# Optimization experiments

Hardware: AMD Instinct MI355X
Metric: run time of the kernel (lower is better)

## Reference

```python
import jax, jax.numpy as jnp
import numpy as np

ALPHA = 0.03
RETURN_WEIGHT = 0.6
SHARPE_WEIGHT = 0.4
WINDOW = 20  # min(20, N//4) == 20 for N = 2**21
N = 2097152


def setup_inputs() -> dict:
    key = jax.random.key(0)
    k1, k2 = jax.random.split(key)
    predictions = jax.random.normal(k1, (N, 1), dtype=jnp.float32)
    returns = jax.random.normal(k2, (N,), dtype=jnp.float32) * 0.02  # daily-return scale
    return {"predictions": predictions, "returns": returns}


def _std(x):
    # torch.std uses the unbiased estimator (ddof=1)
    return jnp.std(x, ddof=1)


def _forward(predictions, returns):
    signals = jnp.tanh(predictions)                 # [N, 1]
    r = returns * signals.squeeze(-1)               # [N] portfolio returns
    n = r.shape[0]

    mean_return = jnp.mean(r)
    std_return = _std(r) + 1e-8
    base_sharpe = mean_return / std_return

    # Rolling std over trailing WINDOW (vectorized form of the python loop):
    # window k covers r[k : k+WINDOW], k in [0, n-WINDOW)
    win = jnp.stack([r[j:n - WINDOW + j] for j in range(WINDOW)], axis=-1)  # [n-W, W]
    rolling_vol = jnp.std(win, axis=-1, ddof=1)
    vol_stability = 1.0 / (_std(rolling_vol) + 1e-6)
    enhanced_sharpe = base_sharpe * (1.0 + 0.1 * vol_stability)

    return_magnitude = jnp.mean(jnp.abs(r))
    positive_frequency = jnp.mean((r > 0).astype(r.dtype))

    dr = r[1:] - r[:-1]
    return_smoothness = 1.0 / (jnp.mean(jnp.abs(dr)) + 1e-6)
    momentum_consistency = jnp.mean(jnp.sign(r[1:]) * jnp.sign(r[:-1]))

    cum = jnp.cumsum(r)
    running_max = jax.lax.cummax(cum, axis=0)
    max_drawdown = jnp.max(running_max - cum)
    drawdown_penalty = jax.nn.relu(max_drawdown - 0.05)

    sorted_r = jnp.sort(r)
    cvar_samples = max(1, int(n * ALPHA))
    cvar = -jnp.mean(sorted_r[:cvar_samples])

    ds = signals[1:] - signals[:-1]
    signal_changes = jnp.mean(jnp.abs(ds))
    signal_smoothness = 1.0 / (signal_changes + 1e-6)

    sharpe_components = (0.4 * enhanced_sharpe
                         + 0.25 * return_magnitude
                         + 0.15 * positive_frequency
                         + 0.1 * momentum_consistency
                         + 0.05 * return_smoothness
                         + 0.05 * signal_smoothness)
    risk_penalties = 0.05 * cvar + 0.02 * drawdown_penalty + 0.01 * signal_changes

    return -(RETURN_WEIGHT * return_magnitude
             + SHARPE_WEIGHT * sharpe_components
             - risk_penalties)


def reference(predictions, returns):
    return _forward(predictions, returns)
```

## Files before the change

kernel.cpp:

```cpp
#include <hip/hip_runtime.h>
#include <math.h>

#define N_TOTAL 2097152
#define WINDOW  20
#define M_ROLL  (N_TOTAL - WINDOW)
#define K_CVAR  62914u

#define BS      512
#define TILE    2048
#define TPB     4
#define SPAN    (TILE * TPB)
#define NB_MAIN (N_TOTAL / SPAN)
#define NBINS   1024
#define CB      1024

#define FPSCALE     2097152.0f
#define INV_FPSCALE (1.0 / 2097152.0)
#define CNT_SHIFT   42

#define ACC_OFF  0
#define HG_OFF   128
#define DDT_OFF  8320
#define ZERO_BYTES 8320

__device__ __forceinline__ unsigned ordkey(float f) {
    unsigned b = __float_as_uint(f);
    return (b & 0x80000000u) ? ~b : (b | 0x80000000u);
}
__device__ __forceinline__ float inv_ordkey(unsigned u) {
    return __uint_as_float((u & 0x80000000u) ? (u ^ 0x80000000u) : ~u);
}
__device__ __forceinline__ float sgnf(float x) {
    return (x > 0.f) ? 1.f : ((x < 0.f) ? -1.f : 0.f);
}
__device__ __forceinline__ float fast_tanh(float x) {
    float ax = fabsf(x);
    float e = __expf(2.0f * ax);
    float t = 1.0f - 2.0f * __builtin_amdgcn_rcpf(e + 1.0f);
    return copysignf(t, x);
}
__device__ __forceinline__ unsigned long long encode_r(float r) {
    float fv = fminf(fmaxf(r + 0.5f, 0.f), 0.9999995f);
    return (1ull << CNT_SHIFT) | (unsigned long long)(unsigned)__float2int_rn(fv * FPSCALE);
}

__global__ __launch_bounds__(BS, 2) void k_main(const float* __restrict__ pred,
                                                const float* __restrict__ ret,
                                                double* __restrict__ acc,
                                                unsigned long long* __restrict__ hg,
                                                double* __restrict__ ddt)
{
    __shared__ __align__(16) float sh_r[TILE + 24];
    __shared__ __align__(16) float sh_s[TILE + 8];
    __shared__ unsigned long long lh[NBINS];
    __shared__ float sred[8][9];
    __shared__ float4 stup[8];

    const int tid = threadIdx.x;
    const int blockStart = blockIdx.x * SPAN;
    const int t4 = tid * 4;

    for (int b = tid; b < NBINS; b += BS) lh[b] = 0ull;

    float sum_r = 0.f, sum_r2 = 0.f, sum_ab = 0.f, cnt_p = 0.f;
    float sum_adr = 0.f, sum_sgn = 0.f, sum_ads = 0.f, vsum = 0.f, vsqr = 0.f;
    double bS = 0.0, bMP = 0.0, bMN = 0.0, bDD = 0.0;

    float4 p4 = *(const float4*)(pred + blockStart + t4);
    float4 q4 = *(const float4*)(ret  + blockStart + t4);

    for (int tt = 0; tt < TPB; ++tt) {
        const int tileStart = blockStart + tt * TILE;

        float sg0 = fast_tanh(p4.x), sg1 = fast_tanh(p4.y);
        float sg2 = fast_tanh(p4.z), sg3 = fast_tanh(p4.w);
        float rr0 = q4.x * sg0, rr1 = q4.y * sg1, rr2 = q4.z * sg2, rr3 = q4.w * sg3;
        *(float4*)&sh_r[4 + t4] = make_float4(rr0, rr1, rr2, rr3);
        *(float4*)&sh_s[4 + t4] = make_float4(sg0, sg1, sg2, sg3);

        if (tid < 6) {
            int k = (tid == 0) ? 0 : (TILE + 4 * tid);
            int g = tileStart + k - 4;
            float4 hp = make_float4(0.f, 0.f, 0.f, 0.f), hq = hp;
            if (g >= 0 && g + 3 < N_TOTAL) {
                hp = *(const float4*)(pred + g);
                hq = *(const float4*)(ret + g);
            }
            float h0 = fast_tanh(hp.x), h1 = fast_tanh(hp.y);
            float h2 = fast_tanh(hp.z), h3 = fast_tanh(hp.w);
            *(float4*)&sh_r[k] = make_float4(hq.x * h0, hq.y * h1, hq.z * h2, hq.w * h3);
            if (tid == 0) *(float4*)&sh_s[0] = make_float4(h0, h1, h2, h3);
        }
        __syncthreads();

        if (tt + 1 < TPB) {
            p4 = *(const float4*)(pred + tileStart + TILE + t4);
            q4 = *(const float4*)(ret  + tileStart + TILE + t4);
        }

        const int k0 = 4 + t4;
        const int iBase = tileStart + t4;

        float4 wv1 = *(float4*)&sh_r[k0 + 4];
        float4 wv2 = *(float4*)&sh_r[k0 + 8];
        float4 wv3 = *(float4*)&sh_r[k0 + 12];
        float4 wv4 = *(float4*)&sh_r[k0 + 16];
        float4 wv5 = *(float4*)&sh_r[k0 + 20];
        float rm1 = sh_r[k0 - 1];
        float sm1 = sh_s[k0 - 1];

        float t_r  = rr0 + rr1 + rr2 + rr3;
        float t_r2 = rr0*rr0 + rr1*rr1 + rr2*rr2 + rr3*rr3;
        sum_r  += t_r;
        sum_r2 += t_r2;
        sum_ab += fabsf(rr0) + fabsf(rr1) + fabsf(rr2) + fabsf(rr3);
        cnt_p  += ((rr0 > 0.f) ? 1.f : 0.f) + ((rr1 > 0.f) ? 1.f : 0.f)
                + ((rr2 > 0.f) ? 1.f : 0.f) + ((rr3 > 0.f) ? 1.f : 0.f);
        sum_adr += fabsf(rr1 - rr0) + fabsf(rr2 - rr1) + fabsf(rr3 - rr2);
        sum_sgn += sgnf(rr1)*sgnf(rr0) + sgnf(rr2)*sgnf(rr1) + sgnf(rr3)*sgnf(rr2);
        sum_ads += fabsf(sg1 - sg0) + fabsf(sg2 - sg1) + fabsf(sg3 - sg2);
        if (iBase >= 1) {
            sum_adr += fabsf(rr0 - rm1);
            sum_sgn += sgnf(rr0) * sgnf(rm1);
            sum_ads += fabsf(sg0 - sm1);
        }

        atomicAdd(&lh[ordkey(rr0) >> 22], encode_r(rr0));
        atomicAdd(&lh[ordkey(rr1) >> 22], encode_r(rr1));
        atomicAdd(&lh[ordkey(rr2) >> 22], encode_r(rr2));
        atomicAdd(&lh[ordkey(rr3) >> 22], encode_r(rr3));

        {
            float ws = t_r, wq = t_r2;
            ws += wv1.x + wv1.y + wv1.z + wv1.w;
            wq += wv1.x*wv1.x + wv1.y*wv1.y + wv1.z*wv1.z + wv1.w*wv1.w;
            ws += wv2.x + wv2.y + wv2.z + wv2.w;
            wq += wv2.x*wv2.x + wv2.y*wv2.y + wv2.z*wv2.z + wv2.w*wv2.w;
            ws += wv3.x + wv3.y + wv3.z + wv3.w;
            wq += wv3.x*wv3.x + wv3.y*wv3.y + wv3.z*wv3.z + wv3.w*wv3.w;
            ws += wv4.x + wv4.y + wv4.z + wv4.w;
            wq += wv4.x*wv4.x + wv4.y*wv4.y + wv4.z*wv4.z + wv4.w*wv4.w;

            if (iBase + 0 < M_ROLL) {
                float var = fmaxf((wq - ws*ws*(1.0f/WINDOW)) * (1.0f/(WINDOW-1)), 0.f);
                vsum += sqrtf(var); vsqr += var;
            }
            ws += wv5.x - rr0; wq += wv5.x*wv5.x - rr0*rr0;
            if (iBase + 1 < M_ROLL) {
                float var = fmaxf((wq - ws*ws*(1.0f/WINDOW)) * (1.0f/(WINDOW-1)), 0.f);
                vsum += sqrtf(var); vsqr += var;
            }
            ws += wv5.y - rr1; wq += wv5.y*wv5.y - rr1*rr1;
            if (iBase + 2 < M_ROLL) {
                float var = fmaxf((wq - ws*ws*(1.0f/WINDOW)) * (1.0f/(WINDOW-1)), 0.f);
                vsum += sqrtf(var); vsqr += var;
            }
            ws += wv5.z - rr2; wq += wv5.z*wv5.z - rr2*rr2;
            if (iBase + 3 < M_ROLL) {
                float var = fmaxf((wq - ws*ws*(1.0f/WINDOW)) * (1.0f/(WINDOW-1)), 0.f);
                vsum += sqrtf(var); vsqr += var;
            }
        }

        float tS = rr0, tMP = rr0, tMN = rr0, tDD = 0.f;
        tS += rr1; tMP = fmaxf(tMP, tS); tMN = fminf(tMN, tS); tDD = fmaxf(tDD, tMP - tS);
        tS += rr2; tMP = fmaxf(tMP, tS); tMN = fminf(tMN, tS); tDD = fmaxf(tDD, tMP - tS);
        tS += rr3; tMP = fmaxf(tMP, tS); tMN = fminf(tMN, tS); tDD = fmaxf(tDD, tMP - tS);
        for (int off = 1; off < 64; off <<= 1) {
            float oS  = __shfl_down(tS,  off);
            float oMP = __shfl_down(tMP, off);
            float oMN = __shfl_down(tMN, off);
            float oDD = __shfl_down(tDD, off);
            float nDD = fmaxf(fmaxf(tDD, oDD), tMP - (tS + oMN));
            float nMP = fmaxf(tMP, tS + oMP);
            float nMN = fminf(tMN, tS + oMN);
            tS += oS; tMP = nMP; tMN = nMN; tDD = nDD;
        }
        if ((tid & 63) == 0) stup[tid >> 6] = make_float4(tS, tMP, tMN, tDD);
        __syncthreads();

        if (tid == 0) {
            for (int w = 0; w < 8; ++w) {
                float4 b = stup[w];
                if (tt == 0 && w == 0) { bS = b.x; bMP = b.y; bMN = b.z; bDD = b.w; }
                else {
                    double nDD = fmax(fmax(bDD, (double)b.w), bMP - (bS + (double)b.z));
                    double nMP = fmax(bMP, bS + (double)b.y);
                    double nMN = fmin(bMN, bS + (double)b.z);
                    bS += (double)b.x; bMP = nMP; bMN = nMN; bDD = nDD;
                }
            }
        }
    }

    for (int off = 1; off < 64; off <<= 1) {
        sum_r  += __shfl_down(sum_r,  off); sum_r2 += __shfl_down(sum_r2, off);
        sum_ab += __shfl_down(sum_ab, off); cnt_p  += __shfl_down(cnt_p,  off);
        sum_adr+= __shfl_down(sum_adr,off); sum_sgn+= __shfl_down(sum_sgn,off);
        sum_ads+= __shfl_down(sum_ads,off); vsum   += __shfl_down(vsum,   off);
        vsqr   += __shfl_down(vsqr,   off);
    }
    int wv = tid >> 6;
    if ((tid & 63) == 0) {
        sred[wv][0]=sum_r;  sred[wv][1]=sum_r2; sred[wv][2]=sum_ab;
        sred[wv][3]=cnt_p;  sred[wv][4]=sum_adr; sred[wv][5]=sum_sgn;
        sred[wv][6]=sum_ads; sred[wv][7]=vsum;   sred[wv][8]=vsqr;
    }
    __syncthreads();

    if (tid < 9) {
        float tot = 0.f;
        for (int w = 0; w < 8; ++w) tot += sred[w][tid];
        atomicAdd(&acc[tid], (double)tot);
    }
    if (tid == 0) {
        double2* dd2 = (double2*)ddt;
        dd2[2 * blockIdx.x]     = make_double2(bS, bMP);
        dd2[2 * blockIdx.x + 1] = make_double2(bMN, bDD);
    }
    for (int b = tid; b < NBINS; b += BS) {
        unsigned long long v = lh[b];
        if (v) atomicAdd(&hg[b], v);
    }
}

__global__ __launch_bounds__(CB) void k_combine(const double* __restrict__ acc,
                                                const unsigned long long* __restrict__ hg,
                                                const double* __restrict__ ddt,
                                                float* __restrict__ out)
{
    __shared__ double dS[NB_MAIN], dMP[NB_MAIN], dMN[NB_MAIN], dDD[NB_MAIN];
    __shared__ double dBS[CB];
    __shared__ unsigned scn[CB];
    __shared__ int s_edge;
    __shared__ unsigned s_cbelow, s_ce;

    const int t = threadIdx.x;

    if (t < NB_MAIN) {
        const double2* dd2 = (const double2*)ddt;
        double2 a0 = dd2[2 * t], a1 = dd2[2 * t + 1];
        dS[t] = a0.x; dMP[t] = a0.y; dMN[t] = a1.x; dDD[t] = a1.y;
    }
    __syncthreads();
    for (int off = 1; off < NB_MAIN; off <<= 1) {
        if (t < NB_MAIN && (t & (2 * off - 1)) == 0) {
            double aS=dS[t], aMP=dMP[t], aMN=dMN[t], aDD=dDD[t];
            double bS=dS[t+off], bMP=dMP[t+off], bMN=dMN[t+off], bDD=dDD[t+off];
            dDD[t] = fmax(fmax(aDD, bDD), aMP - (aS + bMN));
            dMP[t] = fmax(aMP, aS + bMP);
            dMN[t] = fmin(aMN, aS + bMN);
            dS[t]  = aS + bS;
        }
        __syncthreads();
    }

    unsigned long long h = hg[t];
    unsigned cnt = (unsigned)(h >> CNT_SHIFT);
    double sum_bin = (double)(long long)(h & ((1ull << CNT_SHIFT) - 1ull)) * INV_FPSCALE
                   - 0.5 * (double)cnt;
    scn[t] = cnt;
    __syncthreads();
    for (int off = 1; off < CB; off <<= 1) {
        unsigned y = (t >= off) ? scn[t - off] : 0u;
        __syncthreads();
        scn[t] += y;
        __syncthreads();
    }
    unsigned incl = scn[t], excl = incl - cnt;
    if (excl < K_CVAR && incl >= K_CVAR) { s_edge = t; s_cbelow = excl; s_ce = cnt; }
    __syncthreads();
    const int be = s_edge;
    const unsigned cb = s_cbelow, ce = s_ce;

    dBS[t] = (t < be) ? sum_bin : 0.0;
    __syncthreads();
    for (int off = CB / 2; off >= 1; off >>= 1) {
        if (t < off) dBS[t] += dBS[t + off];
        __syncthreads();
    }

    if (t == 0) {
        double n = (double)N_TOTAL;
        double S1 = acc[0], S2 = acc[1], S3 = acc[2], S4 = acc[3];
        double S5 = acc[4], S6 = acc[5], S7 = acc[6], V1 = acc[7], V2 = acc[8];

        double mean_r = S1 / n;
        double var_r = (S2 - S1 * S1 / n) / (n - 1.0);
        if (var_r < 0.0) var_r = 0.0;
        double std_r = sqrt(var_r) + 1e-8;
        double base_sharpe = mean_r / std_r;

        double m = (double)M_ROLL;
        double var_v = (V2 - V1 * V1 / m) / (m - 1.0);
        if (var_v < 0.0) var_v = 0.0;
        double vs = 1.0 / (sqrt(var_v) + 1e-6);
        double es = base_sharpe * (1.0 + 0.1 * vs);

        double rm = S3 / n;
        double pf = S4 / n;
        double rs = 1.0 / (S5 / (n - 1.0) + 1e-6);
        double mc = S6 / (n - 1.0);
        double dd = fmax(dDD[0], 0.0);
        double ddp = dd - 0.05; if (ddp < 0.0) ddp = 0.0;
        double sc = S7 / (n - 1.0);
        double ss = 1.0 / (sc + 1e-6);

        double bsum = dBS[0];
        double mneed = (double)(K_CVAR - cb);
        double elo = (double)inv_ordkey(((unsigned)be) << 22);
        double ehi = (double)inv_ordkey(((unsigned)(be + 1)) << 22);
        double edgev = elo + (mneed / (2.0 * (double)(ce > 0u ? ce : 1u))) * (ehi - elo);
        double cvar = -(bsum + mneed * edgev) / (double)K_CVAR;

        double SC = 0.4 * es + 0.25 * rm + 0.15 * pf + 0.1 * mc + 0.05 * rs + 0.05 * ss;
        double RP = 0.05 * cvar + 0.02 * ddp + 0.01 * sc;
        out[0] = (float)(-(0.6 * rm + 0.4 * SC - RP));
    }
}

extern "C" void kernel_launch(void* const* d_in, const int* in_sizes, int n_in,
                              void* d_out, int out_size, void* d_ws, size_t ws_size,
                              hipStream_t stream)
{
    const float* pred = (const float*)d_in[0];
    const float* ret  = (const float*)d_in[1];
    char* ws = (char*)d_ws;
    double*             acc = (double*)(ws + ACC_OFF);
    unsigned long long* hg  = (unsigned long long*)(ws + HG_OFF);
    double*             ddt = (double*)(ws + DDT_OFF);

    hipMemsetAsync(ws, 0, ZERO_BYTES, stream);
    k_main<<<NB_MAIN, BS, 0, stream>>>(pred, ret, acc, hg, ddt);
    k_combine<<<1, CB, 0, stream>>>(acc, hg, ddt, (float*)d_out);
}
```

Measured before the change: 87.80 us.

## Fuse combine into main kernel via last-block counter and replicate histograms

Removes the separate single-block combine kernel: each block writes per-block partial sums and scan tuples, and the last block to finish (detected by an atomic counter) performs the final reductions with wave shuffles. Local shared-memory histograms are split into 4 sub-copies and the global histogram into 4 copies to reduce atomic contention. The tile count per block is halved, doubling the grid to 512 blocks, with launch bounds raised to 4. This saves a kernel launch and serial combine latency, at the cost of more shared memory, more global histogram traffic, and a threadfence/counter tail.

Result: slower. 141.6 us (+61.3%).

```diff
diff --git a/kernel.cpp b/kernel.cpp
--- a/kernel.cpp
+++ b/kernel.cpp
@@ -8,20 +8,23 @@
 
 #define BS      512
 #define TILE    2048
-#define TPB     4
+#define TPB     2
 #define SPAN    (TILE * TPB)
 #define NB_MAIN (N_TOTAL / SPAN)
 #define NBINS   1024
-#define CB      1024
+#define NSUB    4
+#define NGCOPY  4
 
 #define FPSCALE     2097152.0f
 #define INV_FPSCALE (1.0 / 2097152.0)
 #define CNT_SHIFT   42
-
-#define ACC_OFF  0
-#define HG_OFF   128
-#define DDT_OFF  8320
-#define ZERO_BYTES 8320
+#define SUM_MASK    ((1ull << CNT_SHIFT) - 1ull)
+
+#define HG_OFF   0
+#define CTR_OFF  32768
+#define ZERO_BYTES 32772
+#define DDT_OFF  32800
+#define PBS_OFF  49184
 
 __device__ __forceinline__ unsigned ordkey(float f) {
     unsigned b = __float_as_uint(f);
@@ -44,23 +47,34 @@
     return (1ull << CNT_SHIFT) | (unsigned long long)(unsigned)__float2int_rn(fv * FPSCALE);
 }
 
-__global__ __launch_bounds__(BS, 2) void k_main(const float* __restrict__ pred,
+__global__ __launch_bounds__(BS, 4) void k_main(const float* __restrict__ pred,
                                                 const float* __restrict__ ret,
-                                                double* __restrict__ acc,
                                                 unsigned long long* __restrict__ hg,
-                                                double* __restrict__ ddt)
+                                                unsigned* __restrict__ ctr,
+                                                double* __restrict__ ddt,
+                                                float* __restrict__ pbs,
+                                                float* __restrict__ out)
 {
     __shared__ __align__(16) float sh_r[TILE + 24];
     __shared__ __align__(16) float sh_s[TILE + 8];
-    __shared__ unsigned long long lh[NBINS];
+    __shared__ unsigned long long lh[NSUB][NBINS];
     __shared__ float sred[8][9];
     __shared__ float4 stup[8];
+    __shared__ double s_dd[8][4];
+    __shared__ double s_sc[8][9];
+    __shared__ double s_ds[8];
+    __shared__ unsigned s_wt[8];
+    __shared__ int s_edge;
+    __shared__ unsigned s_cb, s_ce;
+    __shared__ int s_lastflag;
 
     const int tid = threadIdx.x;
+    const int lane = tid & 63, wid = tid >> 6;
     const int blockStart = blockIdx.x * SPAN;
     const int t4 = tid * 4;
-
-    for (int b = tid; b < NBINS; b += BS) lh[b] = 0ull;
+    const int sub = (tid >> 4) & (NSUB - 1);
+
+    for (int b = tid; b < NSUB * NBINS; b += BS) ((unsigned long long*)lh)[b] = 0ull;
 
     float sum_r = 0.f, sum_r2 = 0.f, sum_ab = 0.f, cnt_p = 0.f;
     float sum_adr = 0.f, sum_sgn = 0.f, sum_ads = 0.f, vsum = 0.f, vsqr = 0.f;
@@ -125,10 +139,10 @@
             sum_ads += fabsf(sg0 - sm1);
         }
 
-        atomicAdd(&lh[ordkey(rr0) >> 22], encode_r(rr0));
-        atomicAdd(&lh[ordkey(rr1) >> 22], encode_r(rr1));
-        atomicAdd(&lh[ordkey(rr2) >> 22], encode_r(rr2));
-        atomicAdd(&lh[ordkey(rr3) >> 22], encode_r(rr3));
+        atomicAdd(&lh[sub][ordkey(rr0) >> 22], encode_r(rr0));
+        atomicAdd(&lh[sub][ordkey(rr1) >> 22], encode_r(rr1));
+        atomicAdd(&lh[sub][ordkey(rr2) >> 22], encode_r(rr2));
+        atomicAdd(&lh[sub][ordkey(rr3) >> 22], encode_r(rr3));
 
         {
             float ws = t_r, wq = t_r2;
@@ -176,7 +190,7 @@
             float nMN = fminf(tMN, tS + oMN);
             tS += oS; tMP = nMP; tMN = nMN; tDD = nDD;
         }
-        if ((tid & 63) == 0) stup[tid >> 6] = make_float4(tS, tMP, tMN, tDD);
+        if (lane == 0) stup[wid] = make_float4(tS, tMP, tMN, tDD);
         __syncthreads();
 
         if (tid == 0) {
@@ -200,91 +214,124 @@
         sum_ads+= __shfl_down(sum_ads,off); vsum   += __shfl_down(vsum,   off);
         vsqr   += __shfl_down(vsqr,   off);
     }
-    int wv = tid >> 6;
-    if ((tid & 63) == 0) {
-        sred[wv][0]=sum_r;  sred[wv][1]=sum_r2; sred[wv][2]=sum_ab;
-        sred[wv][3]=cnt_p;  sred[wv][4]=sum_adr; sred[wv][5]=sum_sgn;
-        sred[wv][6]=sum_ads; sred[wv][7]=vsum;   sred[wv][8]=vsqr;
+    if (lane == 0) {
+        sred[wid][0]=sum_r;  sred[wid][1]=sum_r2; sred[wid][2]=sum_ab;
+        sred[wid][3]=cnt_p;  sred[wid][4]=sum_adr; sred[wid][5]=sum_sgn;
+        sred[wid][6]=sum_ads; sred[wid][7]=vsum;   sred[wid][8]=vsqr;
     }
     __syncthreads();
 
     if (tid < 9) {
         float tot = 0.f;
         for (int w = 0; w < 8; ++w) tot += sred[w][tid];
-        atomicAdd(&acc[tid], (double)tot);
+        pbs[blockIdx.x * 12 + tid] = tot;
     }
     if (tid == 0) {
         double2* dd2 = (double2*)ddt;
         dd2[2 * blockIdx.x]     = make_double2(bS, bMP);
         dd2[2 * blockIdx.x + 1] = make_double2(bMN, bDD);
     }
-    for (int b = tid; b < NBINS; b += BS) {
-        unsigned long long v = lh[b];
-        if (v) atomicAdd(&hg[b], v);
-    }
-}
-
-__global__ __launch_bounds__(CB) void k_combine(const double* __restrict__ acc,
-                                                const unsigned long long* __restrict__ hg,
-                                                const double* __restrict__ ddt,
-                                                float* __restrict__ out)
-{
-    __shared__ double dS[NB_MAIN], dMP[NB_MAIN], dMN[NB_MAIN], dDD[NB_MAIN];
-    __shared__ double dBS[CB];
-    __shared__ unsigned scn[CB];
-    __shared__ int s_edge;
-    __shared__ unsigned s_cbelow, s_ce;
-
-    const int t = threadIdx.x;
-
-    if (t < NB_MAIN) {
+    {
+        unsigned long long* gh = hg + (blockIdx.x & (NGCOPY - 1)) * NBINS;
+        for (int b = tid; b < NBINS; b += BS) {
+            unsigned long long v = lh[0][b] + lh[1][b] + lh[2][b] + lh[3][b];
+            if (v) atomicAdd(&gh[b], v);
+        }
+    }
+
+    __threadfence();
+    __syncthreads();
+    if (tid == 0) {
+        unsigned old = atomicAdd(ctr, 1u);
+        s_lastflag = (old == NB_MAIN - 1) ? 1 : 0;
+    }
+    __syncthreads();
+    if (!s_lastflag) return;
+    __threadfence();
+
+    double S, MP, MN, DD;
+    {
         const double2* dd2 = (const double2*)ddt;
-        double2 a0 = dd2[2 * t], a1 = dd2[2 * t + 1];
-        dS[t] = a0.x; dMP[t] = a0.y; dMN[t] = a1.x; dDD[t] = a1.y;
-    }
-    __syncthreads();
-    for (int off = 1; off < NB_MAIN; off <<= 1) {
-        if (t < NB_MAIN && (t & (2 * off - 1)) == 0) {
-            double aS=dS[t], aMP=dMP[t], aMN=dMN[t], aDD=dDD[t];
-            double bS=dS[t+off], bMP=dMP[t+off], bMN=dMN[t+off], bDD=dDD[t+off];
-            dDD[t] = fmax(fmax(aDD, bDD), aMP - (aS + bMN));
-            dMP[t] = fmax(aMP, aS + bMP);
-            dMN[t] = fmin(aMN, aS + bMN);
-            dS[t]  = aS + bS;
-        }
-        __syncthreads();
-    }
-
-    unsigned long long h = hg[t];
-    unsigned cnt = (unsigned)(h >> CNT_SHIFT);
-    double sum_bin = (double)(long long)(h & ((1ull << CNT_SHIFT) - 1ull)) * INV_FPSCALE
-                   - 0.5 * (double)cnt;
-    scn[t] = cnt;
-    __syncthreads();
-    for (int off = 1; off < CB; off <<= 1) {
-        unsigned y = (t >= off) ? scn[t - off] : 0u;
-        __syncthreads();
-        scn[t] += y;
-        __syncthreads();
-    }
-    unsigned incl = scn[t], excl = incl - cnt;
-    if (excl < K_CVAR && incl >= K_CVAR) { s_edge = t; s_cbelow = excl; s_ce = cnt; }
+        double2 a0 = dd2[2 * tid], a1 = dd2[2 * tid + 1];
+        S = a0.x; MP = a0.y; MN = a1.x; DD = a1.y;
+        for (int off = 1; off < 64; off <<= 1) {
+            double oS  = __shfl_down(S,  off);
+            double oMP = __shfl_down(MP, off);
+            double oMN = __shfl_down(MN, off);
+            double oDD = __shfl_down(DD, off);
+            double nDD = fmax(fmax(DD, oDD), MP - (S + oMN));
+            double nMP = fmax(MP, S + oMP);
+            double nMN = fmin(MN, S + oMN);
+            S += oS; MP = nMP; MN = nMN; DD = nDD;
+        }
+        if (lane == 0) { s_dd[wid][0]=S; s_dd[wid][1]=MP; s_dd[wid][2]=MN; s_dd[wid][3]=DD; }
+    }
+    {
+        const float* pb = pbs + tid * 12;
+        double d0=pb[0],d1=pb[1],d2=pb[2],d3=pb[3],d4=pb[4],d5=pb[5],d6=pb[6],d7=pb[7],d8=pb[8];
+        for (int off = 1; off < 64; off <<= 1) {
+            d0+=__shfl_down(d0,off); d1+=__shfl_down(d1,off); d2+=__shfl_down(d2,off);
+            d3+=__shfl_down(d3,off); d4+=__shfl_down(d4,off); d5+=__shfl_down(d5,off);
+            d6+=__shfl_down(d6,off); d7+=__shfl_down(d7,off); d8+=__shfl_down(d8,off);
+        }
+        if (lane == 0) {
+            s_sc[wid][0]=d0; s_sc[wid][1]=d1; s_sc[wid][2]=d2; s_sc[wid][3]=d3;
+            s_sc[wid][4]=d4; s_sc[wid][5]=d5; s_sc[wid][6]=d6; s_sc[wid][7]=d7; s_sc[wid][8]=d8;
+        }
+    }
+    int b0 = 2 * tid, b1 = 2 * tid + 1;
+    unsigned cnt0 = 0, cnt1 = 0;
+    long long fs0 = 0, fs1 = 0;
+    for (int c = 0; c < NGCOPY; ++c) {
+        unsigned long long h0 = hg[c * NBINS + b0];
+        unsigned long long h1 = hg[c * NBINS + b1];
+        cnt0 += (unsigned)(h0 >> CNT_SHIFT); fs0 += (long long)(h0 & SUM_MASK);
+        cnt1 += (unsigned)(h1 >> CNT_SHIFT); fs1 += (long long)(h1 & SUM_MASK);
+    }
+    double sum0 = (double)fs0 * INV_FPSCALE - 0.5 * (double)cnt0;
+    double sum1 = (double)fs1 * INV_FPSCALE - 0.5 * (double)cnt1;
+    unsigned cntt = cnt0 + cnt1;
+    unsigned v = cntt;
+    for (int off = 1; off < 64; off <<= 1) {
+        unsigned y = __shfl_up(v, off);
+        if (lane >= off) v += y;
+    }
+    if (lane == 63) s_wt[wid] = v;
+    __syncthreads();
+    unsigned woff = 0;
+    for (int w = 0; w < wid; ++w) woff += s_wt[w];
+    unsigned incl = v + woff, excl = incl - cntt;
+    if (excl < K_CVAR && excl + cnt0 >= K_CVAR)      { s_edge = b0; s_cb = excl;        s_ce = cnt0; }
+    else if (excl + cnt0 < K_CVAR && incl >= K_CVAR) { s_edge = b1; s_cb = excl + cnt0; s_ce = cnt1; }
     __syncthreads();
     const int be = s_edge;
-    const unsigned cb = s_cbelow, ce = s_ce;
-
-    dBS[t] = (t < be) ? sum_bin : 0.0;
-    __syncthreads();
-    for (int off = CB / 2; off >= 1; off >>= 1) {
-        if (t < off) dBS[t] += dBS[t + off];
-        __syncthreads();
-    }
-
-    if (t == 0) {
+    const unsigned cb = s_cb, ce = s_ce;
+
+    double part = 0.0;
+    if (b0 < be) part += sum0;
+    if (b1 < be) part += sum1;
+    for (int off = 1; off < 64; off <<= 1) part += __shfl_down(part, off);
+    if (lane == 0) s_ds[wid] = part;
+    __syncthreads();
+
+    if (tid == 0) {
+        double gS = s_dd[0][0], gMP = s_dd[0][1], gMN = s_dd[0][2], gDD = s_dd[0][3];
+        for (int w = 1; w < 8; ++w) {
+            double xS = s_dd[w][0], xMP = s_dd[w][1], xMN = s_dd[w][2], xDD = s_dd[w][3];
+            double nDD = fmax(fmax(gDD, xDD), gMP - (gS + xMN));
+            double nMP = fmax(gMP, gS + xMP);
+            double nMN = fmin(gMN, gS + xMN);
+            gS += xS; gMP = nMP; gMN = nMN; gDD = nDD;
+        }
+        double S1=0,S2=0,S3=0,S4=0,S5=0,S6=0,S7=0,V1=0,V2=0;
+        for (int w = 0; w < 8; ++w) {
+            S1+=s_sc[w][0]; S2+=s_sc[w][1]; S3+=s_sc[w][2]; S4+=s_sc[w][3];
+            S5+=s_sc[w][4]; S6+=s_sc[w][5]; S7+=s_sc[w][6]; V1+=s_sc[w][7]; V2+=s_sc[w][8];
+        }
+        double bsum = 0.0;
+        for (int w = 0; w < 8; ++w) bsum += s_ds[w];
+
         double n = (double)N_TOTAL;
-        double S1 = acc[0], S2 = acc[1], S3 = acc[2], S4 = acc[3];
-        double S5 = acc[4], S6 = acc[5], S7 = acc[6], V1 = acc[7], V2 = acc[8];
-
         double mean_r = S1 / n;
         double var_r = (S2 - S1 * S1 / n) / (n - 1.0);
         if (var_r < 0.0) var_r = 0.0;
@@ -301,12 +348,11 @@
         double pf = S4 / n;
         double rs = 1.0 / (S5 / (n - 1.0) + 1e-6);
         double mc = S6 / (n - 1.0);
-        double dd = fmax(dDD[0], 0.0);
+        double dd = fmax(gDD, 0.0);
         double ddp = dd - 0.05; if (ddp < 0.0) ddp = 0.0;
         double sc = S7 / (n - 1.0);
         double ss = 1.0 / (sc + 1e-6);
 
-        double bsum = dBS[0];
         double mneed = (double)(K_CVAR - cb);
         double elo = (double)inv_ordkey(((unsigned)be) << 22);
         double ehi = (double)inv_ordkey(((unsigned)(be + 1)) << 22);
@@ -326,11 +372,11 @@
     const float* pred = (const float*)d_in[0];
     const float* ret  = (const float*)d_in[1];
     char* ws = (char*)d_ws;
-    double*             acc = (double*)(ws + ACC_OFF);
     unsigned long long* hg  = (unsigned long long*)(ws + HG_OFF);
+    unsigned*           ctr = (unsigned*)(ws + CTR_OFF);
     double*             ddt = (double*)(ws + DDT_OFF);
+    float*              pbs = (float*)(ws + PBS_OFF);
 
     hipMemsetAsync(ws, 0, ZERO_BYTES, stream);
-    k_main<<<NB_MAIN, BS, 0, stream>>>(pred, ret, acc, hg, ddt);
-    k_combine<<<1, CB, 0, stream>>>(acc, hg, ddt, (float*)d_out);
-}
+    k_main<<<NB_MAIN, BS, 0, stream>>>(pred, ret, hg, ctr, ddt, pbs, (float*)d_out);
+}
```

## Reduce atomic contention with sub-histograms, histogram copies, and per-block partial sums

Applied to the files above, without the earlier changes.

Halves the tiles per block, which doubles the block count to 512. Each block now keeps two shared-memory sub-histograms, selected by half-wavefront, to spread LDS atomic conflicts. Each block flushes into one of four global histogram copies to cut global atomic contention. The nine scalar sums are no longer sent as global double atomics; each block writes its partials to a buffer, and the combine kernel reduces them with shuffles. The cost is more shared memory per block, a larger memset, and extra reduction work in the single-block combine kernel.

New measurement: 87.19 us. No clear change (-0.7%).

```diff
diff --git a/kernel.cpp b/kernel.cpp
--- a/kernel.cpp
+++ b/kernel.cpp
@@ -8,20 +8,23 @@
 
 #define BS      512
 #define TILE    2048
-#define TPB     4
+#define TPB     2
 #define SPAN    (TILE * TPB)
 #define NB_MAIN (N_TOTAL / SPAN)
 #define NBINS   1024
+#define NSUB    2
+#define NGCOPY  4
 #define CB      1024
 
 #define FPSCALE     2097152.0f
 #define INV_FPSCALE (1.0 / 2097152.0)
 #define CNT_SHIFT   42
-
-#define ACC_OFF  0
-#define HG_OFF   128
-#define DDT_OFF  8320
-#define ZERO_BYTES 8320
+#define SUM_MASK    ((1ull << CNT_SHIFT) - 1ull)
+
+#define HG_OFF   0
+#define ZERO_BYTES 32768
+#define DDT_OFF  32768
+#define PBS_OFF  49152
 
 __device__ __forceinline__ unsigned ordkey(float f) {
     unsigned b = __float_as_uint(f);
@@ -46,21 +49,23 @@
 
 __global__ __launch_bounds__(BS, 2) void k_main(const float* __restrict__ pred,
                                                 const float* __restrict__ ret,
-                                                double* __restrict__ acc,
                                                 unsigned long long* __restrict__ hg,
-                                                double* __restrict__ ddt)
+                                                double* __restrict__ ddt,
+                                                float* __restrict__ pbs)
 {
     __shared__ __align__(16) float sh_r[TILE + 24];
     __shared__ __align__(16) float sh_s[TILE + 8];
-    __shared__ unsigned long long lh[NBINS];
+    __shared__ unsigned long long lh[NSUB][NBINS];
     __shared__ float sred[8][9];
     __shared__ float4 stup[8];
 
     const int tid = threadIdx.x;
+    const int lane = tid & 63, wid = tid >> 6;
     const int blockStart = blockIdx.x * SPAN;
     const int t4 = tid * 4;
-
-    for (int b = tid; b < NBINS; b += BS) lh[b] = 0ull;
+    const int sub = (tid >> 5) & (NSUB - 1);
+
+    for (int b = tid; b < NSUB * NBINS; b += BS) ((unsigned long long*)lh)[b] = 0ull;
 
     float sum_r = 0.f, sum_r2 = 0.f, sum_ab = 0.f, cnt_p = 0.f;
     float sum_adr = 0.f, sum_sgn = 0.f, sum_ads = 0.f, vsum = 0.f, vsqr = 0.f;
@@ -125,10 +130,10 @@
             sum_ads += fabsf(sg0 - sm1);
         }
 
-        atomicAdd(&lh[ordkey(rr0) >> 22], encode_r(rr0));
-        atomicAdd(&lh[ordkey(rr1) >> 22], encode_r(rr1));
-        atomicAdd(&lh[ordkey(rr2) >> 22], encode_r(rr2));
-        atomicAdd(&lh[ordkey(rr3) >> 22], encode_r(rr3));
+        atomicAdd(&lh[sub][ordkey(rr0) >> 22], encode_r(rr0));
+        atomicAdd(&lh[sub][ordkey(rr1) >> 22], encode_r(rr1));
+        atomicAdd(&lh[sub][ordkey(rr2) >> 22], encode_r(rr2));
+        atomicAdd(&lh[sub][ordkey(rr3) >> 22], encode_r(rr3));
 
         {
             float ws = t_r, wq = t_r2;
@@ -176,7 +181,7 @@
             float nMN = fminf(tMN, tS + oMN);
             tS += oS; tMP = nMP; tMN = nMN; tDD = nDD;
         }
-        if ((tid & 63) == 0) stup[tid >> 6] = make_float4(tS, tMP, tMN, tDD);
+        if (lane == 0) stup[wid] = make_float4(tS, tMP, tMN, tDD);
         __syncthreads();
 
         if (tid == 0) {
@@ -200,42 +205,46 @@
         sum_ads+= __shfl_down(sum_ads,off); vsum   += __shfl_down(vsum,   off);
         vsqr   += __shfl_down(vsqr,   off);
     }
-    int wv = tid >> 6;
-    if ((tid & 63) == 0) {
-        sred[wv][0]=sum_r;  sred[wv][1]=sum_r2; sred[wv][2]=sum_ab;
-        sred[wv][3]=cnt_p;  sred[wv][4]=sum_adr; sred[wv][5]=sum_sgn;
-        sred[wv][6]=sum_ads; sred[wv][7]=vsum;   sred[wv][8]=vsqr;
+    if (lane == 0) {
+        sred[wid][0]=sum_r;  sred[wid][1]=sum_r2; sred[wid][2]=sum_ab;
+        sred[wid][3]=cnt_p;  sred[wid][4]=sum_adr; sred[wid][5]=sum_sgn;
+        sred[wid][6]=sum_ads; sred[wid][7]=vsum;   sred[wid][8]=vsqr;
     }
     __syncthreads();
 
     if (tid < 9) {
         float tot = 0.f;
         for (int w = 0; w < 8; ++w) tot += sred[w][tid];
-        atomicAdd(&acc[tid], (double)tot);
+        pbs[blockIdx.x * 12 + tid] = tot;
     }
     if (tid == 0) {
         double2* dd2 = (double2*)ddt;
         dd2[2 * blockIdx.x]     = make_double2(bS, bMP);
         dd2[2 * blockIdx.x + 1] = make_double2(bMN, bDD);
     }
-    for (int b = tid; b < NBINS; b += BS) {
-        unsigned long long v = lh[b];
-        if (v) atomicAdd(&hg[b], v);
-    }
-}
-
-__global__ __launch_bounds__(CB) void k_combine(const double* __restrict__ acc,
-                                                const unsigned long long* __restrict__ hg,
+    {
+        unsigned long long* gh = hg + (blockIdx.x & (NGCOPY - 1)) * NBINS;
+        for (int b = tid; b < NBINS; b += BS) {
+            unsigned long long v = lh[0][b] + lh[1][b];
+            if (v) atomicAdd(&gh[b], v);
+        }
+    }
+}
+
+__global__ __launch_bounds__(CB) void k_combine(const unsigned long long* __restrict__ hg,
                                                 const double* __restrict__ ddt,
+                                                const float* __restrict__ pbs,
                                                 float* __restrict__ out)
 {
     __shared__ double dS[NB_MAIN], dMP[NB_MAIN], dMN[NB_MAIN], dDD[NB_MAIN];
+    __shared__ double s_sc[16][9];
     __shared__ double dBS[CB];
     __shared__ unsigned scn[CB];
     __shared__ int s_edge;
-    __shared__ unsigned s_cbelow, s_ce;
+    __shared__ unsigned s_cb, s_ce;
 
     const int t = threadIdx.x;
+    const int lane = t & 63, wid = t >> 6;
 
     if (t < NB_MAIN) {
         const double2* dd2 = (const double2*)ddt;
@@ -255,10 +264,32 @@
         __syncthreads();
     }
 
-    unsigned long long h = hg[t];
-    unsigned cnt = (unsigned)(h >> CNT_SHIFT);
-    double sum_bin = (double)(long long)(h & ((1ull << CNT_SHIFT) - 1ull)) * INV_FPSCALE
-                   - 0.5 * (double)cnt;
+    {
+        double d0=0,d1=0,d2=0,d3=0,d4=0,d5=0,d6=0,d7=0,d8=0;
+        if (t < NB_MAIN) {
+            const float* pb = pbs + t * 12;
+            d0=pb[0]; d1=pb[1]; d2=pb[2]; d3=pb[3]; d4=pb[4];
+            d5=pb[5]; d6=pb[6]; d7=pb[7]; d8=pb[8];
+        }
+        for (int off = 1; off < 64; off <<= 1) {
+            d0+=__shfl_down(d0,off); d1+=__shfl_down(d1,off); d2+=__shfl_down(d2,off);
+            d3+=__shfl_down(d3,off); d4+=__shfl_down(d4,off); d5+=__shfl_down(d5,off);
+            d6+=__shfl_down(d6,off); d7+=__shfl_down(d7,off); d8+=__shfl_down(d8,off);
+        }
+        if (lane == 0) {
+            s_sc[wid][0]=d0; s_sc[wid][1]=d1; s_sc[wid][2]=d2; s_sc[wid][3]=d3;
+            s_sc[wid][4]=d4; s_sc[wid][5]=d5; s_sc[wid][6]=d6; s_sc[wid][7]=d7; s_sc[wid][8]=d8;
+        }
+    }
+
+    unsigned cnt = 0;
+    long long fs = 0;
+    for (int c = 0; c < NGCOPY; ++c) {
+        unsigned long long h = hg[c * NBINS + t];
+        cnt += (unsigned)(h >> CNT_SHIFT);
+        fs  += (long long)(h & SUM_MASK);
+    }
+    double sum_bin = (double)fs * INV_FPSCALE - 0.5 * (double)cnt;
     scn[t] = cnt;
     __syncthreads();
     for (int off = 1; off < CB; off <<= 1) {
@@ -268,10 +299,10 @@
         __syncthreads();
     }
     unsigned incl = scn[t], excl = incl - cnt;
-    if (excl < K_CVAR && incl >= K_CVAR) { s_edge = t; s_cbelow = excl; s_ce = cnt; }
+    if (excl < K_CVAR && incl >= K_CVAR) { s_edge = t; s_cb = excl; s_ce = cnt; }
     __syncthreads();
     const int be = s_edge;
-    const unsigned cb = s_cbelow, ce = s_ce;
+    const unsigned cb = s_cb, ce = s_ce;
 
     dBS[t] = (t < be) ? sum_bin : 0.0;
     __syncthreads();
@@ -281,10 +312,12 @@
     }
 
     if (t == 0) {
+        double S1=0,S2=0,S3=0,S4=0,S5=0,S6=0,S7=0,V1=0,V2=0;
+        for (int w = 0; w < 16; ++w) {
+            S1+=s_sc[w][0]; S2+=s_sc[w][1]; S3+=s_sc[w][2]; S4+=s_sc[w][3];
+            S5+=s_sc[w][4]; S6+=s_sc[w][5]; S7+=s_sc[w][6]; V1+=s_sc[w][7]; V2+=s_sc[w][8];
+        }
         double n = (double)N_TOTAL;
-        double S1 = acc[0], S2 = acc[1], S3 = acc[2], S4 = acc[3];
-        double S5 = acc[4], S6 = acc[5], S7 = acc[6], V1 = acc[7], V2 = acc[8];
-
         double mean_r = S1 / n;
         double var_r = (S2 - S1 * S1 / n) / (n - 1.0);
         if (var_r < 0.0) var_r = 0.0;
@@ -326,11 +359,11 @@
     const float* pred = (const float*)d_in[0];
     const float* ret  = (const float*)d_in[1];
     char* ws = (char*)d_ws;
-    double*             acc = (double*)(ws + ACC_OFF);
     unsigned long long* hg  = (unsigned long long*)(ws + HG_OFF);
     double*             ddt = (double*)(ws + DDT_OFF);
+    float*              pbs = (float*)(ws + PBS_OFF);
 
     hipMemsetAsync(ws, 0, ZERO_BYTES, stream);
-    k_main<<<NB_MAIN, BS, 0, stream>>>(pred, ret, acc, hg, ddt);
-    k_combine<<<1, CB, 0, stream>>>(acc, hg, ddt, (float*)d_out);
-}
+    k_main<<<NB_MAIN, BS, 0, stream>>>(pred, ret, hg, ddt, pbs);
+    k_combine<<<1, CB, 0, stream>>>(hg, ddt, pbs, (float*)d_out);
+}
```
